# Optimization experiments

Hardware: AMD Instinct MI355X
Metric: run time of the kernel (lower is better)

## Reference

```python
import jax, jax.numpy as jnp
import numpy as np

NUM_HEADS = 8
NEG_INF = -2**32 + 1  # matches the TF code's masking constant


def setup_inputs() -> dict:
    key = jax.random.key(0)
    ks = jax.random.split(key, 12)
    B, L, D_IN, D_MODEL = 2, 2048, 256, 256
    s = 1.0 / np.sqrt(D_IN)
    return {
        "queries": jax.random.normal(ks[0], (B, L, D_IN), jnp.float32),
        "keys": jax.random.normal(ks[1], (B, L, D_IN), jnp.float32),
        "values": jax.random.normal(ks[2], (B, L, D_IN), jnp.float32),
        "key_mask": jax.random.randint(ks[3], (B, L, 1), 0, 2, jnp.int32),
        "Wq": jax.random.normal(ks[4], (D_IN, D_MODEL), jnp.float32) * s,
        "bq": jnp.zeros((D_MODEL,), jnp.float32),
        "Wk": jax.random.normal(ks[5], (D_IN, D_MODEL), jnp.float32) * s,
        "bk": jnp.zeros((D_MODEL,), jnp.float32),
        "Wv": jax.random.normal(ks[6], (D_IN, D_MODEL), jnp.float32) * s,
        "bv": jnp.zeros((D_MODEL,), jnp.float32),
        "Wo": jax.random.normal(ks[7], (D_MODEL, D_IN), jnp.float32) * s,
        "bo": jnp.zeros((D_IN,), jnp.float32),
    }


def reference(queries, keys, values, key_mask, Wq, bq, Wk, bk, Wv, bv, Wo, bo):
    B, Lq, _ = queries.shape
    Lk = keys.shape[1]
    h = NUM_HEADS
    d_model = Wq.shape[1]
    depth = d_model // h

    Q = queries @ Wq + bq  # [B, Lq, d_model]
    K = keys @ Wk + bk     # [B, Lk, d_model]
    V = values @ Wv + bv   # [B, Lk, d_model]

    # split heads: contiguous chunks of size depth along feature dim
    Qh = Q.reshape(B, Lq, h, depth)
    Kh = K.reshape(B, Lk, h, depth)
    Vh = V.reshape(B, Lk, h, depth)

    scores = jnp.einsum("bqhd,bkhd->bhqk", Qh, Kh) / jnp.sqrt(
        jnp.asarray(depth, jnp.float32)
    )  # [B, h, Lq, Lk]

    # key_mask: [B, Lk, 1] -> broadcast over heads and query positions
    mask = (key_mask[:, None, :, 0] != 0)[:, :, None, :]  # [B, 1, 1, Lk]
    scores = jnp.where(mask, scores, jnp.asarray(NEG_INF, scores.dtype))

    attn = jax.nn.softmax(scores, axis=-1)  # dropout is identity at inference
    out = jnp.einsum("bhqk,bkhd->bqhd", attn, Vh).reshape(B, Lq, d_model)
    return out @ Wo + bo  # [B, Lq, input_dim]
```

## Files before the change

### kernel.cpp

```cpp
#include <hip/hip_runtime.h>

#define Bn 2
#define Ln 2048
#define DIN 256
#define Hn 8
#define DEPTH 32
#define SCALE 0.17677669529663687f
#define NEGC (-4294967296.0f)

typedef _Float16 f16;
typedef _Float16 h8 __attribute__((ext_vector_type(8)));
typedef _Float16 h4 __attribute__((ext_vector_type(4)));
typedef float f4 __attribute__((ext_vector_type(4)));

#define WLS 264


__global__ __launch_bounds__(256) void proj_gemm(
    const float* __restrict__ Xq, const float* __restrict__ Xk, const float* __restrict__ Xv,
    const float* __restrict__ Wq, const float* __restrict__ Wk, const float* __restrict__ Wv,
    const float* __restrict__ bq, const float* __restrict__ bk, const float* __restrict__ bv,
    f16* __restrict__ Qb, f16* __restrict__ Kb, f16* __restrict__ Vt)
{
    __shared__ f16 Wl[64 * WLS];
    const int p = blockIdx.z;
    const float* X = p == 0 ? Xq : p == 1 ? Xk : Xv;
    const float* W = p == 0 ? Wq : p == 1 ? Wk : Wv;
    const float* bias = p == 0 ? bq : p == 1 ? bk : bv;

    const int t = threadIdx.x, w = t >> 6, lane = t & 63;
    const int l15 = lane & 15, quad = lane >> 4;
    const int n0 = blockIdx.y * 64;

    {
        const int nl = t & 63, kb = t >> 6;
        for (int kk = 0; kk < 64; ++kk) {
            const int k = kk * 4 + kb;
            Wl[nl * WLS + k] = (f16)W[(size_t)k * DIN + n0 + nl];
        }
    }
    __syncthreads();

    const int m0w = blockIdx.x * 128 + w * 32;
    const float* A0 = X + (size_t)(m0w + l15) * DIN;
    const float* A1 = X + (size_t)(m0w + 16 + l15) * DIN;

    f4 acc[2][4];
    #pragma unroll
    for (int mi = 0; mi < 2; ++mi)
        #pragma unroll
        for (int tt = 0; tt < 4; ++tt) acc[mi][tt] = (f4){0.f, 0.f, 0.f, 0.f};

    for (int k0 = 0; k0 < DIN; k0 += 32) {
        float4 xa0 = *(const float4*)(A0 + k0 + quad * 8);
        float4 xb0 = *(const float4*)(A0 + k0 + quad * 8 + 4);
        float4 xa1 = *(const float4*)(A1 + k0 + quad * 8);
        float4 xb1 = *(const float4*)(A1 + k0 + quad * 8 + 4);
        h8 af0 = { (f16)xa0.x, (f16)xa0.y, (f16)xa0.z, (f16)xa0.w,
                   (f16)xb0.x, (f16)xb0.y, (f16)xb0.z, (f16)xb0.w };
        h8 af1 = { (f16)xa1.x, (f16)xa1.y, (f16)xa1.z, (f16)xa1.w,
                   (f16)xb1.x, (f16)xb1.y, (f16)xb1.z, (f16)xb1.w };
        #pragma unroll
        for (int tt = 0; tt < 4; ++tt) {
            h8 bf = *(const h8*)(Wl + (tt * 16 + l15) * WLS + k0 + quad * 8);
            acc[0][tt] = __builtin_amdgcn_mfma_f32_16x16x32_f16(af0, bf, acc[0][tt], 0, 0, 0);
            acc[1][tt] = __builtin_amdgcn_mfma_f32_16x16x32_f16(af1, bf, acc[1][tt], 0, 0, 0);
        }
    }
    #pragma unroll
    for (int mi = 0; mi < 2; ++mi)
        #pragma unroll
        for (int tt = 0; tt < 4; ++tt) {
            const int c = n0 + tt * 16 + l15;
            const float bb = bias[c];
            const int h = c >> 5, dd = c & 31;
            #pragma unroll
            for (int r = 0; r < 4; ++r) {
                const int row = m0w + mi * 16 + quad * 4 + r;
                const int b = row >> 11, l = row & (Ln - 1);
                const float v = acc[mi][tt][r] + bb;
                if (p == 0)
                    Qb[(((size_t)(b * Hn + h)) * Ln + l) * DEPTH + dd] = (f16)(v * SCALE);
                else if (p == 1)
                    Kb[(((size_t)(b * Hn + h)) * Ln + l) * DEPTH + dd] = (f16)v;
                else
                    Vt[(((size_t)(b * Hn + h)) * DEPTH + dd) * Ln + l] = (f16)v;
            }
        }
}

__global__ __launch_bounds__(256) void flash_mfma(
    const f16* __restrict__ Qb, const f16* __restrict__ Kb,
    const f16* __restrict__ Vt, const int* __restrict__ mask,
    f16* __restrict__ Ob)
{
    __shared__ float Os[4][32][68];
    __shared__ float lS[4][64];
    const int t = threadIdx.x, w = t >> 6, lane = t & 63;
    const int l15 = lane & 15, quad = lane >> 4;
    const int hb = blockIdx.x;
    const int q0 = blockIdx.y * 64;
    const int b = hb >> 3;
    const f16* Qh = Qb + (size_t)hb * Ln * DEPTH;
    const f16* Kh = Kb + (size_t)hb * Ln * DEPTH;
    const f16* Vh = Vt + (size_t)hb * DEPTH * Ln;
    const int* mrow = mask + b * Ln;
    const int k_base = w * (Ln / 4);

    h8 qf[4];
    #pragma unroll
    for (int qg = 0; qg < 4; ++qg)
        qf[qg] = *(const h8*)(Qh + (size_t)(q0 + qg * 16 + l15) * DEPTH + quad * 8);

    f4 o[2][4];
    #pragma unroll
    for (int i = 0; i < 2; ++i)
        #pragma unroll
        for (int j = 0; j < 4; ++j) o[i][j] = (f4){0.f, 0.f, 0.f, 0.f};
    float l_run[4] = {0.f, 0.f, 0.f, 0.f};

    for (int kt = 0; kt < Ln / 4 / 64; ++kt) {
        const int k0 = k_base + kt * 64;
        #pragma unroll
        for (int tt = 0; tt < 4; ++tt) {
            h8 kf = *(const h8*)(Kh + (size_t)(k0 + tt * 16 + l15) * DEPTH + quad * 8);
            const int4 mk = *(const int4*)(mrow + k0 + tt * 16 + quad * 4);
            f4 bias4 = { mk.x ? 0.f : NEGC, mk.y ? 0.f : NEGC,
                         mk.z ? 0.f : NEGC, mk.w ? 0.f : NEGC };
            h4 va0 = *(const h4*)(Vh + (size_t)l15 * Ln        + k0 + tt * 16 + quad * 4);
            h4 va1 = *(const h4*)(Vh + (size_t)(16 + l15) * Ln + k0 + tt * 16 + quad * 4);
            f4 s[4];
            #pragma unroll
            for (int qg = 0; qg < 4; ++qg)
                s[qg] = __builtin_amdgcn_mfma_f32_16x16x32_f16(kf, qf[qg], bias4, 0, 0, 0);
            #pragma unroll
            for (int qg = 0; qg < 4; ++qg) {
                h4 pf;
                #pragma unroll
                for (int r = 0; r < 4; ++r) {
                    const float pv = __expf(s[qg][r]);
                    l_run[qg] += pv;
                    pf[r] = (f16)pv;
                }
                o[0][qg] = __builtin_amdgcn_mfma_f32_16x16x16f16(va0, pf, o[0][qg], 0, 0, 0);
                o[1][qg] = __builtin_amdgcn_mfma_f32_16x16x16f16(va1, pf, o[1][qg], 0, 0, 0);
            }
        }
    }
    #pragma unroll
    for (int qg = 0; qg < 4; ++qg) {
        l_run[qg] += __shfl_xor(l_run[qg], 16, 64);
        l_run[qg] += __shfl_xor(l_run[qg], 32, 64);
        if (quad == 0) lS[w][qg * 16 + l15] = l_run[qg];
        #pragma unroll
        for (int dg = 0; dg < 2; ++dg)
            #pragma unroll
            for (int r = 0; r < 4; ++r)
                Os[w][dg * 16 + quad * 4 + r][qg * 16 + l15] = o[dg][qg][r];
    }
    __syncthreads();

    {
        const int cq = t & 63, dv = t >> 6;
        const float ls = lS[0][cq] + lS[1][cq] + lS[2][cq] + lS[3][cq];
        const float inv = 1.0f / ls;
        h8 pack;
        #pragma unroll
        for (int i = 0; i < 8; ++i) {
            const int dd = dv * 8 + i;
            const float ov = Os[0][dd][cq] + Os[1][dd][cq] +
                             Os[2][dd][cq] + Os[3][dd][cq];
            pack[i] = (f16)(ov * inv);
        }
        *(h8*)(Ob + ((size_t)hb * Ln + q0 + cq) * DEPTH + dv * 8) = pack;
    }
}

__global__ __launch_bounds__(256) void out_gemm(
    const f16* __restrict__ Ob, const float* __restrict__ Wo,
    const float* __restrict__ bo, float* __restrict__ out)
{
    __shared__ f16 Wl[64 * WLS];
    const int t = threadIdx.x, w = t >> 6, lane = t & 63;
    const int l15 = lane & 15, quad = lane >> 4;
    const int m0 = blockIdx.x * 64 + w * 16;
    const int n0 = blockIdx.y * 64;

    {
        const int nl = t & 63, kb = t >> 6;
        for (int kk = 0; kk < 64; ++kk) {
            const int k = kk * 4 + kb;
            Wl[nl * WLS + k] = (f16)Wo[(size_t)k * DIN + n0 + nl];
        }
    }
    __syncthreads();

    const int rA = m0 + l15, bA = rA >> 11, qA = rA & (Ln - 1);

    f4 acc[4] = {{0.f,0.f,0.f,0.f},{0.f,0.f,0.f,0.f},{0.f,0.f,0.f,0.f},{0.f,0.f,0.f,0.f}};
    for (int k0 = 0; k0 < DIN; k0 += 32) {
        const int h = k0 >> 5;
        h8 af = *(const h8*)(Ob + (((size_t)(bA * Hn + h)) * Ln + qA) * DEPTH + quad * 8);
        #pragma unroll
        for (int tt = 0; tt < 4; ++tt) {
            h8 bf = *(const h8*)(Wl + (tt * 16 + l15) * WLS + k0 + quad * 8);
            acc[tt] = __builtin_amdgcn_mfma_f32_16x16x32_f16(af, bf, acc[tt], 0, 0, 0);
        }
    }
    #pragma unroll
    for (int tt = 0; tt < 4; ++tt) {
        const int c = n0 + tt * 16 + l15;
        const float bb = bo[c];
        #pragma unroll
        for (int r = 0; r < 4; ++r)
            out[(size_t)(m0 + quad * 4 + r) * DIN + c] = acc[tt][r] + bb;
    }
}

#define QT 128
#define KT 32
#define TS 34
#define SST (KT + 1)

__global__ __launch_bounds__(512) void fb_fused_attn(
    const float* __restrict__ Xq, const float* __restrict__ Xk,
    const float* __restrict__ Xv, const int* __restrict__ mask,
    const float* __restrict__ Wq, const float* __restrict__ bq,
    const float* __restrict__ Wk, const float* __restrict__ bk,
    const float* __restrict__ Wv, const float* __restrict__ bv,
    float* __restrict__ out)
{
    __shared__ float Qs[QT * TS];
    __shared__ float Ks[KT * TS];
    __shared__ float Vs[KT * TS];
    __shared__ float Ss[QT * SST];
    __shared__ float mrow[QT], lrow[QT], arow[QT];
    __shared__ int mk[KT];

    const int t = threadIdx.x;
    const int d = t & 31;
    const int rg = t >> 5;
    const int q0 = blockIdx.x * QT;
    const int h = blockIdx.y;
    const int b = blockIdx.z;
    const int hc = h * DEPTH + d;

    {
        const float bqv = bq[hc];
        for (int i = 0; i < 8; ++i) {
            const int r = rg + 16 * i;
            const float* x = Xq + ((size_t)(b * Ln + q0 + r)) * DIN;
            float acc = bqv;
            #pragma unroll 8
            for (int k = 0; k < DIN; ++k) acc = fmaf(x[k], Wq[k * DIN + hc], acc);
            Qs[r * TS + d] = acc * SCALE;
        }
    }
    if (t < QT) { mrow[t] = -INFINITY; lrow[t] = 0.f; }
    float o_acc[8];
    #pragma unroll
    for (int i = 0; i < 8; ++i) o_acc[i] = 0.f;

    const float bkv = bk[hc], bvv = bv[hc];

    for (int kt = 0; kt < Ln / KT; ++kt) {
        const int k0 = kt * KT;
        #pragma unroll
        for (int i = 0; i < 2; ++i) {
            const int r = rg + 16 * i;
            const float* xk = Xk + ((size_t)(b * Ln + k0 + r)) * DIN;
            const float* xv = Xv + ((size_t)(b * Ln + k0 + r)) * DIN;
            float aK = bkv, aV = bvv;
            #pragma unroll 4
            for (int k = 0; k < DIN; ++k) {
                aK = fmaf(xk[k], Wk[k * DIN + hc], aK);
                aV = fmaf(xv[k], Wv[k * DIN + hc], aV);
            }
            Ks[r * TS + d] = aK;
            Vs[r * TS + d] = aV;
        }
        if (t < KT) mk[t] = mask[b * Ln + k0 + t];
        __syncthreads();

        for (int idx = t; idx < QT * KT; idx += 512) {
            const int r = idx >> 5, k = idx & (KT - 1);
            const float2* qv = (const float2*)(Qs + r * TS);
            const float2* kv = (const float2*)(Ks + k * TS);
            float s = 0.f;
            #pragma unroll
            for (int j = 0; j < 16; ++j) {
                float2 a = qv[j], c = kv[j];
                s += a.x * c.x + a.y * c.y;
            }
            Ss[r * SST + k] = mk[k] ? s : NEGC;
        }
        __syncthreads();

        if (t < QT) {
            float tm = -INFINITY;
            #pragma unroll 8
            for (int k = 0; k < KT; ++k) tm = fmaxf(tm, Ss[t * SST + k]);
            const float nm = fmaxf(mrow[t], tm);
            arow[t] = __expf(mrow[t] - nm);
            mrow[t] = nm;
        }
        __syncthreads();

        for (int idx = t; idx < QT * KT; idx += 512) {
            const int r = idx >> 5, k = idx & (KT - 1);
            Ss[r * SST + k] = __expf(Ss[r * SST + k] - mrow[r]);
        }
        __syncthreads();

        if (t < QT) {
            float rs = 0.f;
            #pragma unroll 8
            for (int k = 0; k < KT; ++k) rs += Ss[t * SST + k];
            lrow[t] = arow[t] * lrow[t] + rs;
        }
        #pragma unroll
        for (int i = 0; i < 8; ++i) {
            const int r = rg + 16 * i;
            const float a = arow[r];
            float acc = o_acc[i] * a;
            const float* pr = Ss + r * SST;
            const float* vc = Vs + d;
            #pragma unroll 8
            for (int k = 0; k < KT; ++k) acc = fmaf(pr[k], vc[k * TS], acc);
            o_acc[i] = acc;
        }
        __syncthreads();
    }
    #pragma unroll
    for (int i = 0; i < 8; ++i) {
        const int r = rg + 16 * i;
        out[((size_t)(b * Ln + q0 + r)) * DIN + hc] = o_acc[i] / lrow[r];
    }
}

__global__ __launch_bounds__(256) void fb_out_proj(
    const float* __restrict__ Wo, const float* __restrict__ bo,
    float* __restrict__ out)
{
    __shared__ float xr[4][DIN];
    const int col = threadIdx.x;
    const int r0 = blockIdx.x * 4;
    #pragma unroll
    for (int rr = 0; rr < 4; ++rr)
        xr[rr][col] = out[(size_t)(r0 + rr) * DIN + col];
    __syncthreads();
    const float bb = bo[col];
    float a0 = bb, a1 = bb, a2 = bb, a3 = bb;
    #pragma unroll 4
    for (int k = 0; k < DIN; ++k) {
        const float w = Wo[k * DIN + col];
        a0 = fmaf(xr[0][k], w, a0);
        a1 = fmaf(xr[1][k], w, a1);
        a2 = fmaf(xr[2][k], w, a2);
        a3 = fmaf(xr[3][k], w, a3);
    }
    float* o = out + (size_t)r0 * DIN + col;
    o[0] = a0; o[DIN] = a1; o[2 * DIN] = a2; o[3 * DIN] = a3;
}

extern "C" void kernel_launch(void* const* d_in, const int* in_sizes, int n_in,
                              void* d_out, int out_size, void* d_ws, size_t ws_size,
                              hipStream_t stream) {
    const float* Xq = (const float*)d_in[0];
    const float* Xk = (const float*)d_in[1];
    const float* Xv = (const float*)d_in[2];
    const int* mask = (const int*)d_in[3];
    const float* Wq = (const float*)d_in[4];
    const float* bq = (const float*)d_in[5];
    const float* Wk = (const float*)d_in[6];
    const float* bk = (const float*)d_in[7];
    const float* Wv = (const float*)d_in[8];
    const float* bv = (const float*)d_in[9];
    const float* Wo = (const float*)d_in[10];
    const float* bo = (const float*)d_in[11];
    float* out = (float*)d_out;

    const size_t HB_E = (size_t)Bn * Hn * Ln * DEPTH;
    const size_t need = 3 * HB_E * sizeof(f16);

    if (ws_size >= need) {
        f16* Qb = (f16*)d_ws;
        f16* Kb = Qb + HB_E;
        f16* Vt = Kb + HB_E;
        proj_gemm<<<dim3(Bn * Ln / 128, DIN / 64, 3), 256, 0, stream>>>(
            Xq, Xk, Xv, Wq, Wk, Wv, bq, bk, bv, Qb, Kb, Vt);
        flash_mfma<<<dim3(Bn * Hn, Ln / 64), 256, 0, stream>>>(Qb, Kb, Vt, mask, Qb);
        out_gemm<<<dim3(Bn * Ln / 64, DIN / 64), 256, 0, stream>>>(Qb, Wo, bo, out);
    } else {
        fb_fused_attn<<<dim3(Ln / QT, Hn, Bn), 512, 0, stream>>>(
            Xq, Xk, Xv, mask, Wq, bq, Wk, bk, Wv, bv, out);
        fb_out_proj<<<Bn * Ln / 4, 256, 0, stream>>>(Wo, bo, out);
    }
}
```

Measured before the change: 126.4 us.

## Store Q/K/V/O in MFMA fragment-swizzled layout for contiguous per-lane loads

```diff
diff --git a/kernel.cpp b/kernel.cpp
--- a/kernel.cpp
+++ b/kernel.cpp
@@ -14,13 +14,14 @@
 typedef float f4 __attribute__((ext_vector_type(4)));
 
 #define WLS 264
+#define NG  (Ln / 16)
 
 
 __global__ __launch_bounds__(256) void proj_gemm(
     const float* __restrict__ Xq, const float* __restrict__ Xk, const float* __restrict__ Xv,
     const float* __restrict__ Wq, const float* __restrict__ Wk, const float* __restrict__ Wv,
     const float* __restrict__ bq, const float* __restrict__ bk, const float* __restrict__ bv,
-    f16* __restrict__ Qb, f16* __restrict__ Kb, f16* __restrict__ Vt)
+    f16* __restrict__ Qz, f16* __restrict__ Kz, f16* __restrict__ Vz)
 {
     __shared__ f16 Wl[64 * WLS];
     const int p = blockIdx.z;
@@ -79,20 +80,23 @@
                 const int row = m0w + mi * 16 + quad * 4 + r;
                 const int b = row >> 11, l = row & (Ln - 1);
                 const float v = acc[mi][tt][r] + bb;
+                const size_t hbg = (size_t)(b * Hn + h) * NG + (l >> 4);
                 if (p == 0)
-                    Qb[(((size_t)(b * Hn + h)) * Ln + l) * DEPTH + dd] = (f16)(v * SCALE);
+                    Qz[(hbg * 64 + (dd >> 3) * 16 + (l & 15)) * 8 + (dd & 7)] =
+                        (f16)(v * SCALE);
                 else if (p == 1)
-                    Kb[(((size_t)(b * Hn + h)) * Ln + l) * DEPTH + dd] = (f16)v;
+                    Kz[(hbg * 64 + (dd >> 3) * 16 + (l & 15)) * 8 + (dd & 7)] = (f16)v;
                 else
-                    Vt[(((size_t)(b * Hn + h)) * DEPTH + dd) * Ln + l] = (f16)v;
+                    Vz[((hbg * 2 + (dd >> 4)) * 64 + ((l & 15) >> 2) * 16 + (dd & 15)) * 4
+                       + (l & 3)] = (f16)v;
             }
         }
 }
 
 __global__ __launch_bounds__(256) void flash_mfma(
-    const f16* __restrict__ Qb, const f16* __restrict__ Kb,
-    const f16* __restrict__ Vt, const int* __restrict__ mask,
-    f16* __restrict__ Ob)
+    const f16* __restrict__ Qz, const f16* __restrict__ Kz,
+    const f16* __restrict__ Vz, const int* __restrict__ mask,
+    f16* __restrict__ Oz)
 {
     __shared__ float Os[4][32][68];
     __shared__ float lS[4][64];
@@ -100,17 +104,17 @@
     const int l15 = lane & 15, quad = lane >> 4;
     const int hb = blockIdx.x;
     const int q0 = blockIdx.y * 64;
-    const int b = hb >> 3;
-    const f16* Qh = Qb + (size_t)hb * Ln * DEPTH;
-    const f16* Kh = Kb + (size_t)hb * Ln * DEPTH;
-    const f16* Vh = Vt + (size_t)hb * DEPTH * Ln;
+    const int b = hb >> 3, h = hb & 7;
+    const f16* Qh = Qz + (size_t)hb * NG * 512;
+    const f16* Kh = Kz + (size_t)hb * NG * 512;
+    const f16* Vh = Vz + (size_t)hb * NG * 512;
     const int* mrow = mask + b * Ln;
     const int k_base = w * (Ln / 4);
 
     h8 qf[4];
     #pragma unroll
     for (int qg = 0; qg < 4; ++qg)
-        qf[qg] = *(const h8*)(Qh + (size_t)(q0 + qg * 16 + l15) * DEPTH + quad * 8);
+        qf[qg] = *(const h8*)(Qh + ((size_t)(q0 / 16 + qg) * 64 + lane) * 8);
 
     f4 o[2][4];
     #pragma unroll
@@ -123,12 +127,13 @@
         const int k0 = k_base + kt * 64;
         #pragma unroll
         for (int tt = 0; tt < 4; ++tt) {
-            h8 kf = *(const h8*)(Kh + (size_t)(k0 + tt * 16 + l15) * DEPTH + quad * 8);
-            const int4 mk = *(const int4*)(mrow + k0 + tt * 16 + quad * 4);
+            const int g = (k0 >> 4) + tt;
+            h8 kf = *(const h8*)(Kh + ((size_t)g * 64 + lane) * 8);
+            const int4 mk = *(const int4*)(mrow + g * 16 + quad * 4);
             f4 bias4 = { mk.x ? 0.f : NEGC, mk.y ? 0.f : NEGC,
                          mk.z ? 0.f : NEGC, mk.w ? 0.f : NEGC };
-            h4 va0 = *(const h4*)(Vh + (size_t)l15 * Ln        + k0 + tt * 16 + quad * 4);
-            h4 va1 = *(const h4*)(Vh + (size_t)(16 + l15) * Ln + k0 + tt * 16 + quad * 4);
+            h4 va0 = *(const h4*)(Vh + ((size_t)(g * 2)     * 64 + lane) * 4);
+            h4 va1 = *(const h4*)(Vh + ((size_t)(g * 2 + 1) * 64 + lane) * 4);
             f4 s[4];
             #pragma unroll
             for (int qg = 0; qg < 4; ++qg)
@@ -172,12 +177,13 @@
                              Os[2][dd][cq] + Os[3][dd][cq];
             pack[i] = (f16)(ov * inv);
         }
-        *(h8*)(Ob + ((size_t)hb * Ln + q0 + cq) * DEPTH + dv * 8) = pack;
+        const int gm = b * NG + ((q0 + cq) >> 4);
+        *(h8*)(Oz + (((size_t)gm * 8 + h) * 64 + dv * 16 + (cq & 15)) * 8) = pack;
     }
 }
 
 __global__ __launch_bounds__(256) void out_gemm(
-    const f16* __restrict__ Ob, const float* __restrict__ Wo,
+    const f16* __restrict__ Oz, const float* __restrict__ Wo,
     const float* __restrict__ bo, float* __restrict__ out)
 {
     __shared__ f16 Wl[64 * WLS];
@@ -195,12 +201,12 @@
     }
     __syncthreads();
 
-    const int rA = m0 + l15, bA = rA >> 11, qA = rA & (Ln - 1);
+    const int gm = m0 >> 4;
 
     f4 acc[4] = {{0.f,0.f,0.f,0.f},{0.f,0.f,0.f,0.f},{0.f,0.f,0.f,0.f},{0.f,0.f,0.f,0.f}};
     for (int k0 = 0; k0 < DIN; k0 += 32) {
         const int h = k0 >> 5;
-        h8 af = *(const h8*)(Ob + (((size_t)(bA * Hn + h)) * Ln + qA) * DEPTH + quad * 8);
+        h8 af = *(const h8*)(Oz + (((size_t)gm * 8 + h) * 64 + lane) * 8);
         #pragma unroll
         for (int tt = 0; tt < 4; ++tt) {
             h8 bf = *(const h8*)(Wl + (tt * 16 + l15) * WLS + k0 + quad * 8);
@@ -381,16 +387,17 @@
     float* out = (float*)d_out;
 
     const size_t HB_E = (size_t)Bn * Hn * Ln * DEPTH;
-    const size_t need = 3 * HB_E * sizeof(f16);
+    const size_t need = 4 * HB_E * sizeof(f16);
 
     if (ws_size >= need) {
-        f16* Qb = (f16*)d_ws;
-        f16* Kb = Qb + HB_E;
-        f16* Vt = Kb + HB_E;
+        f16* Qz = (f16*)d_ws;
+        f16* Kz = Qz + HB_E;
+        f16* Vz = Kz + HB_E;
+        f16* Oz = Vz + HB_E;
         proj_gemm<<<dim3(Bn * Ln / 128, DIN / 64, 3), 256, 0, stream>>>(
-            Xq, Xk, Xv, Wq, Wk, Wv, bq, bk, bv, Qb, Kb, Vt);
-        flash_mfma<<<dim3(Bn * Hn, Ln / 64), 256, 0, stream>>>(Qb, Kb, Vt, mask, Qb);
-        out_gemm<<<dim3(Bn * Ln / 64, DIN / 64), 256, 0, stream>>>(Qb, Wo, bo, out);
+            Xq, Xk, Xv, Wq, Wk, Wv, bq, bk, bv, Qz, Kz, Vz);
+        flash_mfma<<<dim3(Bn * Hn, Ln / 64), 256, 0, stream>>>(Qz, Kz, Vz, mask, Oz);
+        out_gemm<<<dim3(Bn * Ln / 64, DIN / 64), 256, 0, stream>>>(Oz, Wo, bo, out);
     } else {
         fb_fused_attn<<<dim3(Ln / QT, Hn, Bn), 512, 0, stream>>>(
             Xq, Xk, Xv, mask, Wq, bq, Wk, bk, Wv, bv, out);
```

Result: faster. 123.9 us (-2.0%).
